# Kernel tuning notes

Measured on AMD Instinct MI355X. Metric: run time of the kernel, lower is better.

The kernel has to match this reference:

```python
import jax, jax.numpy as jnp
import numpy as np

N_NODES = 50000
N_EDGES = 1600000
D_FEAT = 64
N_SCALARS = 4
N_GRAPHS = 64
HIDDEN = 128
OUT = 128


def setup_inputs() -> dict:
    key = jax.random.key(0)
    ks = jax.random.split(key, 8)
    x = jax.random.normal(ks[0], (N_NODES, D_FEAT), dtype=jnp.float32)
    scalars = jax.random.normal(ks[1], (N_GRAPHS, N_SCALARS), dtype=jnp.float32)
    batch = jnp.sort(jax.random.randint(ks[2], (N_NODES,), 0, N_GRAPHS))
    edge_index = jax.random.randint(ks[3], (2, N_EDGES), 0, N_NODES)
    d_in = 2 * (D_FEAT + N_SCALARS)  # 136: EdgeConv-style cat([x_i, x_j - x_i])
    W1 = jax.random.normal(ks[4], (d_in, HIDDEN), dtype=jnp.float32) * (1.0 / np.sqrt(d_in))
    b1 = jnp.zeros((HIDDEN,), dtype=jnp.float32)
    W2 = jax.random.normal(ks[5], (HIDDEN, OUT), dtype=jnp.float32) * (1.0 / np.sqrt(HIDDEN))
    b2 = jnp.zeros((OUT,), dtype=jnp.float32)
    return {"x": x, "scalars": scalars, "batch": batch, "edge_index": edge_index,
            "W1": W1, "b1": b1, "W2": W2, "b2": b2}


def reference(x, scalars, batch, edge_index, W1, b1, W2, b2):
    # _reshape_scalars: gather per-graph scalars to nodes via batch index
    s = scalars[batch]                       # [N, n_scalars]
    h = jnp.concatenate([x, s], axis=-1)     # [N, d_feat + n_scalars]
    src, dst = edge_index[0], edge_index[1]  # edge j -> i (PyG convention)
    h_i = h[dst]                             # target node features [E, F]
    h_j = h[src]                             # source node features [E, F]
    m_in = jnp.concatenate([h_i, h_j - h_i], axis=-1)  # [E, 2F]
    m = jax.nn.relu(m_in @ W1 + b1) @ W2 + b2          # edge MLP [E, OUT]
    out = jax.ops.segment_sum(m, dst, num_segments=x.shape[0])  # add-aggregation
    return out
```

## Files before the change

### kernel.cpp

```cpp
#include <hip/hip_runtime.h>

#define N_NODES   50000
#define N_EDGES   1600000
#define D_FEAT    64
#define N_SCALARS 4
#define HIDDEN    128
#define OUT_DIM   128
#define UV_DIM    256

#define SLICE_SH  6
#define SLICE_N   (1 << SLICE_SH)
#define NSLICE    ((N_NODES + SLICE_N - 1) >> SLICE_SH)
#define CAP       2560
#define DEGMAX    80
#define CAPN      96
#define CAPN_DW   (CAPN / 2)
#define CHUNK     4096
#define SENTINEL  50000

#define N_WAVES   (N_NODES / 16)
#define G1_BLOCKS ((N_WAVES + 3) / 4)
#define BIN_BLOCKS ((N_EDGES + CHUNK - 1) / CHUNK)
#define AGG_BLOCKS (N_NODES / 16)

typedef __attribute__((ext_vector_type(8))) _Float16 half8;
typedef __attribute__((ext_vector_type(2))) _Float16 half2v;
typedef __attribute__((ext_vector_type(4))) float    f32x4;

__device__ __forceinline__ float wf_elem(const float* W1, int k, int j) {
    float wb = W1[(k + 68) * HIDDEN + (j & 127)];
    return (j < HIDDEN) ? (W1[k * HIDDEN + j] - wb) : wb;
}

__device__ __forceinline__ unsigned char f2bf8(float f) {
    unsigned short h = __builtin_bit_cast(unsigned short, (_Float16)f);
    unsigned r = ((unsigned)h + 0x7Fu + ((h >> 8) & 1u)) >> 8;
    return (unsigned char)r;
}

__device__ __forceinline__ half2v bf8lo(unsigned v) {
    return __builtin_bit_cast(half2v, __builtin_amdgcn_perm(0u, v, 0x010C000Cu));
}
__device__ __forceinline__ half2v bf8hi(unsigned v) {
    return __builtin_bit_cast(half2v, __builtin_amdgcn_perm(0u, v, 0x030C020Cu));
}
__device__ __forceinline__ half2v h2bc(unsigned v) {
    return __builtin_bit_cast(half2v, v);
}
__device__ __forceinline__ unsigned h2u(half2v v) {
    return __builtin_bit_cast(unsigned, v);
}

__global__ __launch_bounds__(256) void prep_kernel(
    const float* __restrict__ W1, const float* __restrict__ b1,
    const float* __restrict__ W2, const float* __restrict__ scalars,
    _Float16* __restrict__ WfT, _Float16* __restrict__ W2T,
    float* __restrict__ SG, int* __restrict__ tails,
    unsigned char* __restrict__ Vb8)
{
    const int idx = blockIdx.x * 256 + threadIdx.x;
    {   int j = idx >> 6, k = idx & 63;
        WfT[idx] = (_Float16)wf_elem(W1, k, j); }
    {   int j = idx >> 7, k = idx & 127;
        W2T[idx] = (_Float16)W2[k * OUT_DIM + j]; }
    {   int g = idx >> 8, j = idx & 255;
        float s = (j < HIDDEN) ? b1[j] : 0.f;
        #pragma unroll
        for (int t = 0; t < N_SCALARS; ++t)
            s = fmaf(scalars[g * N_SCALARS + t], wf_elem(W1, D_FEAT + t, j), s);
        SG[idx] = s; }
    if (idx < NSLICE) tails[idx] = 0;
    if (idx < 32)
        ((unsigned*)(Vb8 + (size_t)SENTINEL * HIDDEN))[idx] = 0xFCFCFCFCu;
}

__global__ __launch_bounds__(256) void gemm1_bin(
    const float* __restrict__ x, const int* __restrict__ batch,
    const _Float16* __restrict__ WfT, const float* __restrict__ SG,
    _Float16* __restrict__ Uh, unsigned char* __restrict__ Vb8,
    const int* __restrict__ ei, int* __restrict__ tails,
    unsigned* __restrict__ glist)
{
    __shared__ unsigned buf[CHUNK];
    __shared__ int hist[NSLICE];
    __shared__ int binStart[NSLICE];
    __shared__ int cursor[NSLICE];
    __shared__ int gbase[NSLICE];
    __shared__ int scanTmp[256];

    const int tid = threadIdx.x;

    if (blockIdx.x < G1_BLOCKS) {
        const int wid = (blockIdx.x * 256 + tid) >> 6;
        if (wid >= N_WAVES) return;
        const int lane = tid & 63;
        const int quad = lane >> 4;
        const int l15  = lane & 15;
        const int row0 = wid * 16;

        f32x4 acc[16];
        #pragma unroll
        for (int c = 0; c < 16; ++c) { f32x4 z = {0.f,0.f,0.f,0.f}; acc[c] = z; }

        const float* xrow = x + (row0 + l15) * D_FEAT;
        #pragma unroll
        for (int t = 0; t < 2; ++t) {
            const int k0 = 32 * t + quad * 8;
            float4 a0 = *(const float4*)(xrow + k0);
            float4 a1 = *(const float4*)(xrow + k0 + 4);
            half8 af;
            af[0] = (_Float16)a0.x; af[1] = (_Float16)a0.y;
            af[2] = (_Float16)a0.z; af[3] = (_Float16)a0.w;
            af[4] = (_Float16)a1.x; af[5] = (_Float16)a1.y;
            af[6] = (_Float16)a1.z; af[7] = (_Float16)a1.w;
            #pragma unroll
            for (int c = 0; c < 16; ++c) {
                half8 bf = *(const half8*)(WfT + (c * 16 + l15) * 64 + k0);
                acc[c] = __builtin_amdgcn_mfma_f32_16x16x32_f16(af, bf, acc[c], 0, 0, 0);
            }
        }

        const int gA = batch[row0];
        const int gB = batch[row0 + 15];

        if (gA == gB) {
            const float* SGr = SG + gA * UV_DIM;
            #pragma unroll
            for (int c = 0; c < 16; ++c) {
                const int col = c * 16 + l15;
                const float sg = SGr[col];
                #pragma unroll
                for (int j = 0; j < 4; ++j) {
                    const int n = row0 + quad * 4 + j;
                    float v = acc[c][j] + sg;
                    if (col < HIDDEN) Uh[(n << 7) + col] = (_Float16)v;
                    else              Vb8[(n << 7) + col - HIDDEN] = f2bf8(v);
                }
            }
        } else {
            int bg[4];
            #pragma unroll
            for (int j = 0; j < 4; ++j) bg[j] = batch[row0 + quad * 4 + j];
            #pragma unroll
            for (int c = 0; c < 16; ++c) {
                const int col = c * 16 + l15;
                #pragma unroll
                for (int j = 0; j < 4; ++j) {
                    const int n = row0 + quad * 4 + j;
                    float v = acc[c][j] + SG[bg[j] * UV_DIM + col];
                    if (col < HIDDEN) Uh[(n << 7) + col] = (_Float16)v;
                    else              Vb8[(n << 7) + col - HIDDEN] = f2bf8(v);
                }
            }
        }
        return;
    }

    const int e0  = (blockIdx.x - G1_BLOCKS) * CHUNK;
    const int nE  = min(CHUNK, N_EDGES - e0);

    for (int i = tid; i < NSLICE; i += 256) hist[i] = 0;
    __syncthreads();

    unsigned ent[CHUNK / 256];
    #pragma unroll
    for (int j = 0; j < CHUNK / 256; ++j) {
        int e = e0 + tid + j * 256;
        if (e < N_EDGES) {
            unsigned s = (unsigned)ei[e];
            unsigned d = (unsigned)ei[N_EDGES + e];
            ent[j] = (d << 16) | s;
            atomicAdd(&hist[d >> SLICE_SH], 1);
        } else {
            ent[j] = 0xFFFFFFFFu;
        }
    }
    __syncthreads();

    const int base4 = tid * 4;
    int loc[4];
    int sum = 0;
    #pragma unroll
    for (int k = 0; k < 4; ++k) {
        int b = base4 + k;
        loc[k] = (b < NSLICE) ? hist[b] : 0;
        sum += loc[k];
    }
    scanTmp[tid] = sum;
    __syncthreads();
    for (int d = 1; d < 256; d <<= 1) {
        int v = (tid >= d) ? scanTmp[tid - d] : 0;
        __syncthreads();
        scanTmp[tid] += v;
        __syncthreads();
    }
    int run = (tid == 0) ? 0 : scanTmp[tid - 1];
    #pragma unroll
    for (int k = 0; k < 4; ++k) {
        int b = base4 + k;
        if (b < NSLICE) { binStart[b] = run; cursor[b] = run; run += loc[k]; }
    }
    __syncthreads();

    #pragma unroll
    for (int j = 0; j < CHUNK / 256; ++j) {
        if (ent[j] != 0xFFFFFFFFu) {
            int sl = (int)(ent[j] >> (16 + SLICE_SH));
            int pos = atomicAdd(&cursor[sl], 1);
            buf[pos] = ent[j];
        }
    }
    __syncthreads();

    for (int s = tid; s < NSLICE; s += 256) {
        int c = hist[s];
        if (c > 0) gbase[s] = atomicAdd(&tails[s], c);
    }
    __syncthreads();

    for (int i = tid; i < nE; i += 256) {
        unsigned e = buf[i];
        int sl = (int)(e >> (16 + SLICE_SH));
        int di = gbase[sl] + (i - binStart[sl]);
        if (di < CAP) glist[(size_t)sl * CAP + di] = e;
    }
}

__global__ __launch_bounds__(256) void rebin_kernel(
    const unsigned* __restrict__ glist, const int* __restrict__ tails,
    unsigned short* __restrict__ nlist, int* __restrict__ degN)
{
    __shared__ unsigned short lists[64 * CAPN];
    __shared__ int cur[64];

    const int sl  = blockIdx.x;
    const int tid = threadIdx.x;
    const unsigned* lst = glist + (size_t)sl * CAP;
    const int cnt = min(tails[sl], CAP);

    unsigned* L32 = (unsigned*)lists;
    #pragma unroll
    for (int k = 0; k < (64 * CAPN_DW) / 256; ++k)
        L32[tid + k * 256] = (SENTINEL << 16) | SENTINEL;
    if (tid < 64) cur[tid] = 0;
    __syncthreads();

    for (int i = tid; i < cnt; i += 256) {
        unsigned e = lst[i];
        int b = (e >> 16) & 63;
        int pos = atomicAdd(&cur[b], 1);
        if (pos < DEGMAX) lists[b * CAPN + pos] = (unsigned short)e;
    }
    __syncthreads();

    unsigned* N32 = (unsigned*)nlist + (size_t)sl * (64 * CAPN_DW);
    #pragma unroll
    for (int k = 0; k < (64 * CAPN_DW) / 256; ++k)
        N32[tid + k * 256] = L32[tid + k * 256];

    if (tid < 64) degN[sl * 64 + tid] = min(cur[tid], DEGMAX);
}

__global__ __launch_bounds__(512, 8) void agg_gemm2(
    const unsigned short* __restrict__ nlist, const int* __restrict__ degN,
    const _Float16* __restrict__ Uh, const unsigned char* __restrict__ Vb8,
    const _Float16* __restrict__ W2T, const float* __restrict__ b2,
    float* __restrict__ out)
{
    __shared__ _Float16 aggA[16][136];
    __shared__ int deg16[16];

    const int node0 = blockIdx.x << 4;
    const int tid   = threadIdx.x;
    const int wave  = tid >> 6;
    const int lane  = tid & 63;
    const int g     = lane >> 3;
    const int co    = (lane & 7) * 16;
    const half2v zero = {(_Float16)0, (_Float16)0};

    if (tid < 16) deg16[tid] = min(degN[node0 + tid], DEGMAX);

    const int n0 = node0 + wave * 2;
    const int d0 = min(degN[n0], DEGMAX);
    const int d1 = min(degN[n0 + 1], DEGMAX);
    const int nch = (max(d0, d1) + 7) >> 3;

    const unsigned char* Vbc = Vb8 + co;
    const unsigned short* L0 = nlist + (size_t)n0 * CAPN + g;
    const unsigned short* L1 = L0 + CAPN;

    half2v U0[8], U1[8], A0[8], A1[8];
    {
        const _Float16* up = Uh + (((size_t)n0) << 7) + co;
        uint4 a = *(const uint4*)up;
        uint4 b = *(const uint4*)(up + 8);
        U0[0] = h2bc(a.x); U0[1] = h2bc(a.y);
        U0[2] = h2bc(a.z); U0[3] = h2bc(a.w);
        U0[4] = h2bc(b.x); U0[5] = h2bc(b.y);
        U0[6] = h2bc(b.z); U0[7] = h2bc(b.w);
        uint4 c = *(const uint4*)(up + 128);
        uint4 d = *(const uint4*)(up + 136);
        U1[0] = h2bc(c.x); U1[1] = h2bc(c.y);
        U1[2] = h2bc(c.z); U1[3] = h2bc(c.w);
        U1[4] = h2bc(d.x); U1[5] = h2bc(d.y);
        U1[6] = h2bc(d.z); U1[7] = h2bc(d.w);
        #pragma unroll
        for (int k = 0; k < 8; ++k) { A0[k] = zero; A1[k] = zero; }
    }

    unsigned s0c = L0[0], s1c = L1[0];
    unsigned s0n = L0[8], s1n = L1[8];
    uint4 v0 = *(const uint4*)(Vbc + ((size_t)s0c << 7));
    uint4 v1 = *(const uint4*)(Vbc + ((size_t)s1c << 7));

    for (int ch = 0; ch < nch; ++ch) {
        uint4 v0n = *(const uint4*)(Vbc + ((size_t)s0n << 7));
        uint4 v1n = *(const uint4*)(Vbc + ((size_t)s1n << 7));
        s0n = L0[(ch + 2) * 8];
        s1n = L1[(ch + 2) * 8];

        A0[0] += __builtin_elementwise_max(U0[0] + bf8lo(v0.x), zero);
        A0[1] += __builtin_elementwise_max(U0[1] + bf8hi(v0.x), zero);
        A0[2] += __builtin_elementwise_max(U0[2] + bf8lo(v0.y), zero);
        A0[3] += __builtin_elementwise_max(U0[3] + bf8hi(v0.y), zero);
        A0[4] += __builtin_elementwise_max(U0[4] + bf8lo(v0.z), zero);
        A0[5] += __builtin_elementwise_max(U0[5] + bf8hi(v0.z), zero);
        A0[6] += __builtin_elementwise_max(U0[6] + bf8lo(v0.w), zero);
        A0[7] += __builtin_elementwise_max(U0[7] + bf8hi(v0.w), zero);
        A1[0] += __builtin_elementwise_max(U1[0] + bf8lo(v1.x), zero);
        A1[1] += __builtin_elementwise_max(U1[1] + bf8hi(v1.x), zero);
        A1[2] += __builtin_elementwise_max(U1[2] + bf8lo(v1.y), zero);
        A1[3] += __builtin_elementwise_max(U1[3] + bf8hi(v1.y), zero);
        A1[4] += __builtin_elementwise_max(U1[4] + bf8lo(v1.z), zero);
        A1[5] += __builtin_elementwise_max(U1[5] + bf8hi(v1.z), zero);
        A1[6] += __builtin_elementwise_max(U1[6] + bf8lo(v1.w), zero);
        A1[7] += __builtin_elementwise_max(U1[7] + bf8hi(v1.w), zero);

        v0 = v0n; v1 = v1n;
    }

    #pragma unroll
    for (int k = 0; k < 8; ++k) {
        half2v t0 = A0[k];
        t0 += h2bc((unsigned)__shfl_xor((int)h2u(t0), 8));
        t0 += h2bc((unsigned)__shfl_xor((int)h2u(t0), 16));
        t0 += h2bc((unsigned)__shfl_xor((int)h2u(t0), 32));
        A0[k] = t0;
        half2v t1 = A1[k];
        t1 += h2bc((unsigned)__shfl_xor((int)h2u(t1), 8));
        t1 += h2bc((unsigned)__shfl_xor((int)h2u(t1), 16));
        t1 += h2bc((unsigned)__shfl_xor((int)h2u(t1), 32));
        A1[k] = t1;
    }

    if (lane < 8) {
        _Float16* dst0 = &aggA[wave * 2][co];
        uint4 w0 = { h2u(A0[0]), h2u(A0[1]), h2u(A0[2]), h2u(A0[3]) };
        uint4 w1 = { h2u(A0[4]), h2u(A0[5]), h2u(A0[6]), h2u(A0[7]) };
        *(uint4*)dst0 = w0;
        *(uint4*)(dst0 + 8) = w1;
        _Float16* dst1 = &aggA[wave * 2 + 1][co];
        uint4 w2 = { h2u(A1[0]), h2u(A1[1]), h2u(A1[2]), h2u(A1[3]) };
        uint4 w3 = { h2u(A1[4]), h2u(A1[5]), h2u(A1[6]), h2u(A1[7]) };
        *(uint4*)dst1 = w2;
        *(uint4*)(dst1 + 8) = w3;
    }
    __syncthreads();

    const int quad = lane >> 4;
    const int l15  = lane & 15;
    f32x4 accm = {0.f, 0.f, 0.f, 0.f};
    #pragma unroll
    for (int t = 0; t < 4; ++t) {
        const int k0 = 32 * t + quad * 8;
        half8 af = *(const half8*)&aggA[l15][k0];
        half8 bf = *(const half8*)(W2T + ((wave * 16 + l15) << 7) + k0);
        accm = __builtin_amdgcn_mfma_f32_16x16x32_f16(af, bf, accm, 0, 0, 0);
    }
    int dgj[4];
    #pragma unroll
    for (int j = 0; j < 4; ++j) dgj[j] = deg16[quad * 4 + j];

    const int col = wave * 16 + l15;
    const float bb = b2[col];
    #pragma unroll
    for (int j = 0; j < 4; ++j) {
        const int n = node0 + quad * 4 + j;
        out[(size_t)n * OUT_DIM + col] = accm[j] + bb * (float)dgj[j];
    }
}

extern "C" void kernel_launch(void* const* d_in, const int* in_sizes, int n_in,
                              void* d_out, int out_size, void* d_ws, size_t ws_size,
                              hipStream_t stream)
{
    const float* x       = (const float*)d_in[0];
    const float* scalars = (const float*)d_in[1];
    const int*   batch   = (const int*)d_in[2];
    const int*   ei      = (const int*)d_in[3];
    const float* W1      = (const float*)d_in[4];
    const float* b1      = (const float*)d_in[5];
    const float* W2      = (const float*)d_in[6];
    const float* b2      = (const float*)d_in[7];
    float*       out     = (float*)d_out;

    _Float16*       Uh    = (_Float16*)d_ws;
    unsigned char*  Vb8   = (unsigned char*)(Uh + (size_t)N_NODES * HIDDEN);
    unsigned*       glist = (unsigned*)(Vb8 + (size_t)(N_NODES + 1) * HIDDEN);
    unsigned short* nlist = (unsigned short*)(glist + (size_t)NSLICE * CAP);
    int*            degN  = (int*)(nlist + (size_t)NSLICE * SLICE_N * CAPN);
    _Float16*       WfT   = (_Float16*)(degN + NSLICE * SLICE_N);
    _Float16*       W2T   = WfT + 256 * 64;
    float*          SG    = (float*)(W2T + 128 * 128);
    int*            tails = (int*)(SG + 64 * UV_DIM);

    prep_kernel<<<64, 256, 0, stream>>>(W1, b1, W2, scalars, WfT, W2T, SG, tails, Vb8);

    gemm1_bin<<<G1_BLOCKS + BIN_BLOCKS, 256, 0, stream>>>(
        x, batch, WfT, SG, Uh, Vb8, ei, tails, glist);

    rebin_kernel<<<NSLICE, 256, 0, stream>>>(glist, tails, nlist, degN);

    agg_gemm2<<<AGG_BLOCKS, 512, 0, stream>>>(
        nlist, degN, Uh, Vb8, W2T, b2, out);
}
```

Baseline: 166.1 us.

## Replace global atomic slice tails with per-block staged buckets and histograms

The binning blocks now write each locally sorted chunk straight to a staging buffer, along with per-block histograms and bin starts, instead of reserving space through global atomics on per-slice tails and scattering into fixed-capacity slice lists. The rebin kernel then walks every binning block's segment for its slice. This removes the global atomics, the tails reset and the scattered writes, in exchange for rebin reading a 391x782 metadata matrix and doing short serial per-thread segment loops with poor coalescing. It also drops the CAP overflow truncation, and the resulting edge order can differ.

Result: slower. 172.7 us (+4.0%).

```diff
diff --git a/kernel.cpp b/kernel.cpp
--- a/kernel.cpp
+++ b/kernel.cpp
@@ -11,7 +11,6 @@
 #define SLICE_SH  6
 #define SLICE_N   (1 << SLICE_SH)
 #define NSLICE    ((N_NODES + SLICE_N - 1) >> SLICE_SH)
-#define CAP       2560
 #define DEGMAX    80
 #define CAPN      96
 #define CAPN_DW   (CAPN / 2)
@@ -55,8 +54,7 @@
     const float* __restrict__ W1, const float* __restrict__ b1,
     const float* __restrict__ W2, const float* __restrict__ scalars,
     _Float16* __restrict__ WfT, _Float16* __restrict__ W2T,
-    float* __restrict__ SG, int* __restrict__ tails,
-    unsigned char* __restrict__ Vb8)
+    float* __restrict__ SG, unsigned char* __restrict__ Vb8)
 {
     const int idx = blockIdx.x * 256 + threadIdx.x;
     {   int j = idx >> 6, k = idx & 63;
@@ -69,7 +67,6 @@
         for (int t = 0; t < N_SCALARS; ++t)
             s = fmaf(scalars[g * N_SCALARS + t], wf_elem(W1, D_FEAT + t, j), s);
         SG[idx] = s; }
-    if (idx < NSLICE) tails[idx] = 0;
     if (idx < 32)
         ((unsigned*)(Vb8 + (size_t)SENTINEL * HIDDEN))[idx] = 0xFCFCFCFCu;
 }
@@ -78,14 +75,13 @@
     const float* __restrict__ x, const int* __restrict__ batch,
     const _Float16* __restrict__ WfT, const float* __restrict__ SG,
     _Float16* __restrict__ Uh, unsigned char* __restrict__ Vb8,
-    const int* __restrict__ ei, int* __restrict__ tails,
-    unsigned* __restrict__ glist)
+    const int* __restrict__ ei, unsigned* __restrict__ gstage,
+    int* __restrict__ histM, int* __restrict__ startM)
 {
     __shared__ unsigned buf[CHUNK];
     __shared__ int hist[NSLICE];
     __shared__ int binStart[NSLICE];
     __shared__ int cursor[NSLICE];
-    __shared__ int gbase[NSLICE];
     __shared__ int scanTmp[256];
 
     const int tid = threadIdx.x;
@@ -156,8 +152,8 @@
         return;
     }
 
-    const int e0  = (blockIdx.x - G1_BLOCKS) * CHUNK;
-    const int nE  = min(CHUNK, N_EDGES - e0);
+    const int bb  = blockIdx.x - G1_BLOCKS;
+    const int e0  = bb * CHUNK;
 
     for (int i = tid; i < NSLICE; i += 256) hist[i] = 0;
     __syncthreads();
@@ -212,22 +208,19 @@
     }
     __syncthreads();
 
+    unsigned* gs = gstage + (size_t)bb * CHUNK;
+    #pragma unroll
+    for (int j = 0; j < CHUNK / 256; ++j)
+        gs[tid + j * 256] = buf[tid + j * 256];
     for (int s = tid; s < NSLICE; s += 256) {
-        int c = hist[s];
-        if (c > 0) gbase[s] = atomicAdd(&tails[s], c);
-    }
-    __syncthreads();
-
-    for (int i = tid; i < nE; i += 256) {
-        unsigned e = buf[i];
-        int sl = (int)(e >> (16 + SLICE_SH));
-        int di = gbase[sl] + (i - binStart[sl]);
-        if (di < CAP) glist[(size_t)sl * CAP + di] = e;
+        histM [(size_t)bb * NSLICE + s] = hist[s];
+        startM[(size_t)bb * NSLICE + s] = binStart[s];
     }
 }
 
 __global__ __launch_bounds__(256) void rebin_kernel(
-    const unsigned* __restrict__ glist, const int* __restrict__ tails,
+    const unsigned* __restrict__ gstage, const int* __restrict__ histM,
+    const int* __restrict__ startM,
     unsigned short* __restrict__ nlist, int* __restrict__ degN)
 {
     __shared__ unsigned short lists[64 * CAPN];
@@ -235,8 +228,6 @@
 
     const int sl  = blockIdx.x;
     const int tid = threadIdx.x;
-    const unsigned* lst = glist + (size_t)sl * CAP;
-    const int cnt = min(tails[sl], CAP);
 
     unsigned* L32 = (unsigned*)lists;
     #pragma unroll
@@ -245,11 +236,17 @@
     if (tid < 64) cur[tid] = 0;
     __syncthreads();
 
-    for (int i = tid; i < cnt; i += 256) {
-        unsigned e = lst[i];
-        int b = (e >> 16) & 63;
-        int pos = atomicAdd(&cur[b], 1);
-        if (pos < DEGMAX) lists[b * CAPN + pos] = (unsigned short)e;
+    for (int b = tid; b < BIN_BLOCKS; b += 256) {
+        const int len = histM[(size_t)b * NSLICE + sl];
+        if (len <= 0) continue;
+        const unsigned* seg = gstage + (size_t)b * CHUNK
+                            + startM[(size_t)b * NSLICE + sl];
+        for (int i = 0; i < len; ++i) {
+            unsigned e = seg[i];
+            int nd = (e >> 16) & 63;
+            int pos = atomicAdd(&cur[nd], 1);
+            if (pos < DEGMAX) lists[nd * CAPN + pos] = (unsigned short)e;
+        }
     }
     __syncthreads();
 
@@ -404,22 +401,23 @@
     const float* b2      = (const float*)d_in[7];
     float*       out     = (float*)d_out;
 
-    _Float16*       Uh    = (_Float16*)d_ws;
-    unsigned char*  Vb8   = (unsigned char*)(Uh + (size_t)N_NODES * HIDDEN);
-    unsigned*       glist = (unsigned*)(Vb8 + (size_t)(N_NODES + 1) * HIDDEN);
-    unsigned short* nlist = (unsigned short*)(glist + (size_t)NSLICE * CAP);
-    int*            degN  = (int*)(nlist + (size_t)NSLICE * SLICE_N * CAPN);
-    _Float16*       WfT   = (_Float16*)(degN + NSLICE * SLICE_N);
-    _Float16*       W2T   = WfT + 256 * 64;
-    float*          SG    = (float*)(W2T + 128 * 128);
-    int*            tails = (int*)(SG + 64 * UV_DIM);
-
-    prep_kernel<<<64, 256, 0, stream>>>(W1, b1, W2, scalars, WfT, W2T, SG, tails, Vb8);
+    _Float16*       Uh     = (_Float16*)d_ws;
+    unsigned char*  Vb8    = (unsigned char*)(Uh + (size_t)N_NODES * HIDDEN);
+    unsigned*       gstage = (unsigned*)(Vb8 + (size_t)(N_NODES + 1) * HIDDEN);
+    unsigned short* nlist  = (unsigned short*)(gstage + (size_t)BIN_BLOCKS * CHUNK);
+    int*            degN   = (int*)(nlist + (size_t)NSLICE * SLICE_N * CAPN);
+    int*            histM  = degN + NSLICE * SLICE_N;
+    int*            startM = histM + (size_t)BIN_BLOCKS * NSLICE;
+    _Float16*       WfT    = (_Float16*)(startM + (size_t)BIN_BLOCKS * NSLICE);
+    _Float16*       W2T    = WfT + 256 * 64;
+    float*          SG     = (float*)(W2T + 128 * 128);
+
+    prep_kernel<<<64, 256, 0, stream>>>(W1, b1, W2, scalars, WfT, W2T, SG, Vb8);
 
     gemm1_bin<<<G1_BLOCKS + BIN_BLOCKS, 256, 0, stream>>>(
-        x, batch, WfT, SG, Uh, Vb8, ei, tails, glist);
-
-    rebin_kernel<<<NSLICE, 256, 0, stream>>>(glist, tails, nlist, degN);
+        x, batch, WfT, SG, Uh, Vb8, ei, gstage, histM, startM);
+
+    rebin_kernel<<<NSLICE, 256, 0, stream>>>(gstage, histM, startM, nlist, degN);
 
     agg_gemm2<<<AGG_BLOCKS, 512, 0, stream>>>(
         nlist, degN, Uh, Vb8, W2T, b2, out);
```

## Split edge aggregation into two column-half passes to shrink gather working set

Applied to the files above, without the earlier changes.

The aggregation kernel is split into two launches. Each one gathers only 64 of the 128 hidden columns of the fp8 V table per neighbour, and the first pass stores its partial aggregate to a workspace buffer that the second pass reads back before the GEMM2 MFMA. The aim is to halve the random-gather footprint of Vb8 per pass so each half stays cache-resident. In exchange it adds an extra kernel launch, reads the neighbour lists and degrees twice, writes and reads back an intermediate buffer, and issues narrower 8-byte gathers.

Result: slower. 192.4 us (+15.8%).

```diff
diff --git a/kernel.cpp b/kernel.cpp
--- a/kernel.cpp
+++ b/kernel.cpp
@@ -261,61 +261,46 @@
     if (tid < 64) degN[sl * 64 + tid] = min(cur[tid], DEGMAX);
 }
 
-__global__ __launch_bounds__(512, 8) void agg_gemm2(
+template<int H>
+__device__ __forceinline__ void agg_gather_half(
     const unsigned short* __restrict__ nlist, const int* __restrict__ degN,
     const _Float16* __restrict__ Uh, const unsigned char* __restrict__ Vb8,
-    const _Float16* __restrict__ W2T, const float* __restrict__ b2,
-    float* __restrict__ out)
-{
-    __shared__ _Float16 aggA[16][136];
-    __shared__ int deg16[16];
-
-    const int node0 = blockIdx.x << 4;
-    const int tid   = threadIdx.x;
-    const int wave  = tid >> 6;
-    const int lane  = tid & 63;
-    const int g     = lane >> 3;
-    const int co    = (lane & 7) * 16;
+    int node0, int wave, int lane, half2v A0[4], half2v A1[4])
+{
+    const int g  = lane >> 3;
+    const int co = (lane & 7) * 8;
     const half2v zero = {(_Float16)0, (_Float16)0};
-
-    if (tid < 16) deg16[tid] = min(degN[node0 + tid], DEGMAX);
 
     const int n0 = node0 + wave * 2;
     const int d0 = min(degN[n0], DEGMAX);
     const int d1 = min(degN[n0 + 1], DEGMAX);
     const int nch = (max(d0, d1) + 7) >> 3;
 
-    const unsigned char* Vbc = Vb8 + co;
+    const unsigned char* Vbc = Vb8 + H * 64 + co;
     const unsigned short* L0 = nlist + (size_t)n0 * CAPN + g;
     const unsigned short* L1 = L0 + CAPN;
 
-    half2v U0[8], U1[8], A0[8], A1[8];
+    half2v U0[4], U1[4];
     {
-        const _Float16* up = Uh + (((size_t)n0) << 7) + co;
+        const _Float16* up = Uh + (((size_t)n0) << 7) + H * 64 + co;
         uint4 a = *(const uint4*)up;
-        uint4 b = *(const uint4*)(up + 8);
         U0[0] = h2bc(a.x); U0[1] = h2bc(a.y);
         U0[2] = h2bc(a.z); U0[3] = h2bc(a.w);
-        U0[4] = h2bc(b.x); U0[5] = h2bc(b.y);
-        U0[6] = h2bc(b.z); U0[7] = h2bc(b.w);
         uint4 c = *(const uint4*)(up + 128);
-        uint4 d = *(const uint4*)(up + 136);
         U1[0] = h2bc(c.x); U1[1] = h2bc(c.y);
         U1[2] = h2bc(c.z); U1[3] = h2bc(c.w);
-        U1[4] = h2bc(d.x); U1[5] = h2bc(d.y);
-        U1[6] = h2bc(d.z); U1[7] = h2bc(d.w);
         #pragma unroll
-        for (int k = 0; k < 8; ++k) { A0[k] = zero; A1[k] = zero; }
+        for (int k = 0; k < 4; ++k) { A0[k] = zero; A1[k] = zero; }
     }
 
     unsigned s0c = L0[0], s1c = L1[0];
     unsigned s0n = L0[8], s1n = L1[8];
-    uint4 v0 = *(const uint4*)(Vbc + ((size_t)s0c << 7));
-    uint4 v1 = *(const uint4*)(Vbc + ((size_t)s1c << 7));
+    uint2 v0 = *(const uint2*)(Vbc + ((size_t)s0c << 7));
+    uint2 v1 = *(const uint2*)(Vbc + ((size_t)s1c << 7));
 
     for (int ch = 0; ch < nch; ++ch) {
-        uint4 v0n = *(const uint4*)(Vbc + ((size_t)s0n << 7));
-        uint4 v1n = *(const uint4*)(Vbc + ((size_t)s1n << 7));
+        uint2 v0n = *(const uint2*)(Vbc + ((size_t)s0n << 7));
+        uint2 v1n = *(const uint2*)(Vbc + ((size_t)s1n << 7));
         s0n = L0[(ch + 2) * 8];
         s1n = L1[(ch + 2) * 8];
 
@@ -323,24 +308,16 @@
         A0[1] += __builtin_elementwise_max(U0[1] + bf8hi(v0.x), zero);
         A0[2] += __builtin_elementwise_max(U0[2] + bf8lo(v0.y), zero);
         A0[3] += __builtin_elementwise_max(U0[3] + bf8hi(v0.y), zero);
-        A0[4] += __builtin_elementwise_max(U0[4] + bf8lo(v0.z), zero);
-        A0[5] += __builtin_elementwise_max(U0[5] + bf8hi(v0.z), zero);
-        A0[6] += __builtin_elementwise_max(U0[6] + bf8lo(v0.w), zero);
-        A0[7] += __builtin_elementwise_max(U0[7] + bf8hi(v0.w), zero);
         A1[0] += __builtin_elementwise_max(U1[0] + bf8lo(v1.x), zero);
         A1[1] += __builtin_elementwise_max(U1[1] + bf8hi(v1.x), zero);
         A1[2] += __builtin_elementwise_max(U1[2] + bf8lo(v1.y), zero);
         A1[3] += __builtin_elementwise_max(U1[3] + bf8hi(v1.y), zero);
-        A1[4] += __builtin_elementwise_max(U1[4] + bf8lo(v1.z), zero);
-        A1[5] += __builtin_elementwise_max(U1[5] + bf8hi(v1.z), zero);
-        A1[6] += __builtin_elementwise_max(U1[6] + bf8lo(v1.w), zero);
-        A1[7] += __builtin_elementwise_max(U1[7] + bf8hi(v1.w), zero);
 
         v0 = v0n; v1 = v1n;
     }
 
     #pragma unroll
-    for (int k = 0; k < 8; ++k) {
+    for (int k = 0; k < 4; ++k) {
         half2v t0 = A0[k];
         t0 += h2bc((unsigned)__shfl_xor((int)h2u(t0), 8));
         t0 += h2bc((unsigned)__shfl_xor((int)h2u(t0), 16));
@@ -352,18 +329,62 @@
         t1 += h2bc((unsigned)__shfl_xor((int)h2u(t1), 32));
         A1[k] = t1;
     }
+}
+
+__global__ __launch_bounds__(512, 8) void agg_pass1(
+    const unsigned short* __restrict__ nlist, const int* __restrict__ degN,
+    const _Float16* __restrict__ Uh, const unsigned char* __restrict__ Vb8,
+    _Float16* __restrict__ Pagg)
+{
+    const int node0 = blockIdx.x << 4;
+    const int tid   = threadIdx.x;
+    const int wave  = tid >> 6;
+    const int lane  = tid & 63;
+
+    half2v A0[4], A1[4];
+    agg_gather_half<0>(nlist, degN, Uh, Vb8, node0, wave, lane, A0, A1);
 
     if (lane < 8) {
-        _Float16* dst0 = &aggA[wave * 2][co];
+        const int n0 = node0 + wave * 2;
+        const int co = (lane & 7) * 8;
         uint4 w0 = { h2u(A0[0]), h2u(A0[1]), h2u(A0[2]), h2u(A0[3]) };
-        uint4 w1 = { h2u(A0[4]), h2u(A0[5]), h2u(A0[6]), h2u(A0[7]) };
-        *(uint4*)dst0 = w0;
-        *(uint4*)(dst0 + 8) = w1;
-        _Float16* dst1 = &aggA[wave * 2 + 1][co];
-        uint4 w2 = { h2u(A1[0]), h2u(A1[1]), h2u(A1[2]), h2u(A1[3]) };
-        uint4 w3 = { h2u(A1[4]), h2u(A1[5]), h2u(A1[6]), h2u(A1[7]) };
-        *(uint4*)dst1 = w2;
-        *(uint4*)(dst1 + 8) = w3;
+        uint4 w1 = { h2u(A1[0]), h2u(A1[1]), h2u(A1[2]), h2u(A1[3]) };
+        *(uint4*)(Pagg + (size_t)n0 * 64 + co) = w0;
+        *(uint4*)(Pagg + (size_t)(n0 + 1) * 64 + co) = w1;
+    }
+}
+
+__global__ __launch_bounds__(512, 8) void agg_pass2(
+    const unsigned short* __restrict__ nlist, const int* __restrict__ degN,
+    const _Float16* __restrict__ Uh, const unsigned char* __restrict__ Vb8,
+    const _Float16* __restrict__ Pagg,
+    const _Float16* __restrict__ W2T, const float* __restrict__ b2,
+    float* __restrict__ out)
+{
+    __shared__ _Float16 aggA[16][136];
+    __shared__ int deg16[16];
+
+    const int node0 = blockIdx.x << 4;
+    const int tid   = threadIdx.x;
+    const int wave  = tid >> 6;
+    const int lane  = tid & 63;
+
+    if (tid < 16) deg16[tid] = min(degN[node0 + tid], DEGMAX);
+
+    half2v A0[4], A1[4];
+    agg_gather_half<1>(nlist, degN, Uh, Vb8, node0, wave, lane, A0, A1);
+
+    if (lane < 8) {
+        const int n0 = node0 + wave * 2;
+        const int co = (lane & 7) * 8;
+        uint4 w0 = { h2u(A0[0]), h2u(A0[1]), h2u(A0[2]), h2u(A0[3]) };
+        uint4 w1 = { h2u(A1[0]), h2u(A1[1]), h2u(A1[2]), h2u(A1[3]) };
+        *(uint4*)&aggA[wave * 2][64 + co] = w0;
+        *(uint4*)&aggA[wave * 2 + 1][64 + co] = w1;
+        uint4 p0 = *(const uint4*)(Pagg + (size_t)n0 * 64 + co);
+        uint4 p1 = *(const uint4*)(Pagg + (size_t)(n0 + 1) * 64 + co);
+        *(uint4*)&aggA[wave * 2][co] = p0;
+        *(uint4*)&aggA[wave * 2 + 1][co] = p1;
     }
     __syncthreads();
 
@@ -409,7 +430,8 @@
     unsigned*       glist = (unsigned*)(Vb8 + (size_t)(N_NODES + 1) * HIDDEN);
     unsigned short* nlist = (unsigned short*)(glist + (size_t)NSLICE * CAP);
     int*            degN  = (int*)(nlist + (size_t)NSLICE * SLICE_N * CAPN);
-    _Float16*       WfT   = (_Float16*)(degN + NSLICE * SLICE_N);
+    _Float16*       Pagg  = (_Float16*)(degN + NSLICE * SLICE_N);
+    _Float16*       WfT   = Pagg + (size_t)N_NODES * 64;
     _Float16*       W2T   = WfT + 256 * 64;
     float*          SG    = (float*)(W2T + 128 * 128);
     int*            tails = (int*)(SG + 64 * UV_DIM);
@@ -421,6 +443,8 @@
 
     rebin_kernel<<<NSLICE, 256, 0, stream>>>(glist, tails, nlist, degN);
 
-    agg_gemm2<<<AGG_BLOCKS, 512, 0, stream>>>(
-        nlist, degN, Uh, Vb8, W2T, b2, out);
-}
+    agg_pass1<<<AGG_BLOCKS, 512, 0, stream>>>(nlist, degN, Uh, Vb8, Pagg);
+
+    agg_pass2<<<AGG_BLOCKS, 512, 0, stream>>>(
+        nlist, degN, Uh, Vb8, Pagg, W2T, b2, out);
+}
```

## Split aggregation into two source-range passes for L2 locality of V gathers

Applied to the files above, without the earlier changes.

The rebin kernel now splits each node's neighbor list into a low-source half (src < 25000) and a high-source half, padded to chunk boundaries, and records both degrees. Aggregation runs as two kernels: pass A gathers only the low-half V rows and writes fp16 partial sums to a new workspace buffer, and pass B gathers the high half, adds the partials and does the second GEMM. Each pass touches only half the V table, which is meant to keep the random gathers resident in cache. The cost is an extra launch, a second edge-list scan in rebin, extra chunk padding and the write and read of a fp16 partial-sum buffer. The bin CHUNK size is also doubled.

Result: slower. 191.8 us (+15.5%).

```diff
diff --git a/kernel.cpp b/kernel.cpp
--- a/kernel.cpp
+++ b/kernel.cpp
@@ -15,8 +15,9 @@
 #define DEGMAX    80
 #define CAPN      96
 #define CAPN_DW   (CAPN / 2)
-#define CHUNK     4096
+#define CHUNK     8192
 #define SENTINEL  50000
+#define SRC_HALF  25000
 
 #define N_WAVES   (N_NODES / 16)
 #define G1_BLOCKS ((N_WAVES + 3) / 4)
@@ -228,10 +229,13 @@
 
 __global__ __launch_bounds__(256) void rebin_kernel(
     const unsigned* __restrict__ glist, const int* __restrict__ tails,
-    unsigned short* __restrict__ nlist, int* __restrict__ degN)
+    unsigned short* __restrict__ nlist, int* __restrict__ degN,
+    int* __restrict__ degLoN)
 {
     __shared__ unsigned short lists[64 * CAPN];
     __shared__ int cur[64];
+    __shared__ int lo64[64];
+    __shared__ int base64[64];
 
     const int sl  = blockIdx.x;
     const int tid = threadIdx.x;
@@ -247,9 +251,27 @@
 
     for (int i = tid; i < cnt; i += 256) {
         unsigned e = lst[i];
-        int b = (e >> 16) & 63;
-        int pos = atomicAdd(&cur[b], 1);
-        if (pos < DEGMAX) lists[b * CAPN + pos] = (unsigned short)e;
+        if ((e & 0xFFFFu) < SRC_HALF) {
+            int b = (e >> 16) & 63;
+            int pos = atomicAdd(&cur[b], 1);
+            if (pos < DEGMAX) lists[b * CAPN + pos] = (unsigned short)e;
+        }
+    }
+    __syncthreads();
+    if (tid < 64) {
+        int lo = min(cur[tid], DEGMAX);
+        lo64[tid]   = lo;
+        base64[tid] = (lo + 7) & ~7;
+        cur[tid]    = base64[tid];
+    }
+    __syncthreads();
+    for (int i = tid; i < cnt; i += 256) {
+        unsigned e = lst[i];
+        if ((e & 0xFFFFu) >= SRC_HALF) {
+            int b = (e >> 16) & 63;
+            int pos = atomicAdd(&cur[b], 1);
+            if (pos < CAPN) lists[b * CAPN + pos] = (unsigned short)e;
+        }
     }
     __syncthreads();
 
@@ -258,66 +280,47 @@
     for (int k = 0; k < (64 * CAPN_DW) / 256; ++k)
         N32[tid + k * 256] = L32[tid + k * 256];
 
-    if (tid < 64) degN[sl * 64 + tid] = min(cur[tid], DEGMAX);
-}
-
-__global__ __launch_bounds__(512, 8) void agg_gemm2(
-    const unsigned short* __restrict__ nlist, const int* __restrict__ degN,
-    const _Float16* __restrict__ Uh, const unsigned char* __restrict__ Vb8,
-    const _Float16* __restrict__ W2T, const float* __restrict__ b2,
-    float* __restrict__ out)
-{
-    __shared__ _Float16 aggA[16][136];
-    __shared__ int deg16[16];
-
-    const int node0 = blockIdx.x << 4;
-    const int tid   = threadIdx.x;
-    const int wave  = tid >> 6;
-    const int lane  = tid & 63;
-    const int g     = lane >> 3;
-    const int co    = (lane & 7) * 16;
+    if (tid < 64) {
+        int lo = lo64[tid];
+        int hi = min(cur[tid], CAPN) - base64[tid];
+        degLoN[sl * 64 + tid] = lo;
+        degN  [sl * 64 + tid] = lo + hi;
+    }
+}
+
+__device__ __forceinline__ unsigned sid_at(
+    const unsigned short* L, int base, int nchN, int c)
+{
+    int cc = min(c, max(nchN - 1, 0));
+    unsigned v = L[base + cc * 8];
+    return (c < nchN) ? v : (unsigned)SENTINEL;
+}
+
+__device__ __forceinline__ void agg_gather_seg(
+    const unsigned short* L0, const unsigned short* L1,
+    int base0, int cnt0, int base1, int cnt1,
+    const unsigned char* Vbc,
+    const half2v U0[8], const half2v U1[8],
+    half2v A0[8], half2v A1[8])
+{
     const half2v zero = {(_Float16)0, (_Float16)0};
-
-    if (tid < 16) deg16[tid] = min(degN[node0 + tid], DEGMAX);
-
-    const int n0 = node0 + wave * 2;
-    const int d0 = min(degN[n0], DEGMAX);
-    const int d1 = min(degN[n0 + 1], DEGMAX);
-    const int nch = (max(d0, d1) + 7) >> 3;
-
-    const unsigned char* Vbc = Vb8 + co;
-    const unsigned short* L0 = nlist + (size_t)n0 * CAPN + g;
-    const unsigned short* L1 = L0 + CAPN;
-
-    half2v U0[8], U1[8], A0[8], A1[8];
-    {
-        const _Float16* up = Uh + (((size_t)n0) << 7) + co;
-        uint4 a = *(const uint4*)up;
-        uint4 b = *(const uint4*)(up + 8);
-        U0[0] = h2bc(a.x); U0[1] = h2bc(a.y);
-        U0[2] = h2bc(a.z); U0[3] = h2bc(a.w);
-        U0[4] = h2bc(b.x); U0[5] = h2bc(b.y);
-        U0[6] = h2bc(b.z); U0[7] = h2bc(b.w);
-        uint4 c = *(const uint4*)(up + 128);
-        uint4 d = *(const uint4*)(up + 136);
-        U1[0] = h2bc(c.x); U1[1] = h2bc(c.y);
-        U1[2] = h2bc(c.z); U1[3] = h2bc(c.w);
-        U1[4] = h2bc(d.x); U1[5] = h2bc(d.y);
-        U1[6] = h2bc(d.z); U1[7] = h2bc(d.w);
-        #pragma unroll
-        for (int k = 0; k < 8; ++k) { A0[k] = zero; A1[k] = zero; }
-    }
-
-    unsigned s0c = L0[0], s1c = L1[0];
-    unsigned s0n = L0[8], s1n = L1[8];
+    const int nch0 = (cnt0 + 7) >> 3;
+    const int nch1 = (cnt1 + 7) >> 3;
+    const int nch  = max(nch0, nch1);
+    if (nch == 0) return;
+
+    unsigned s0c = sid_at(L0, base0, nch0, 0);
+    unsigned s1c = sid_at(L1, base1, nch1, 0);
+    unsigned s0n = sid_at(L0, base0, nch0, 1);
+    unsigned s1n = sid_at(L1, base1, nch1, 1);
     uint4 v0 = *(const uint4*)(Vbc + ((size_t)s0c << 7));
     uint4 v1 = *(const uint4*)(Vbc + ((size_t)s1c << 7));
 
     for (int ch = 0; ch < nch; ++ch) {
         uint4 v0n = *(const uint4*)(Vbc + ((size_t)s0n << 7));
         uint4 v1n = *(const uint4*)(Vbc + ((size_t)s1n << 7));
-        s0n = L0[(ch + 2) * 8];
-        s1n = L1[(ch + 2) * 8];
+        s0n = sid_at(L0, base0, nch0, ch + 2);
+        s1n = sid_at(L1, base1, nch1, ch + 2);
 
         A0[0] += __builtin_elementwise_max(U0[0] + bf8lo(v0.x), zero);
         A0[1] += __builtin_elementwise_max(U0[1] + bf8hi(v0.x), zero);
@@ -338,7 +341,10 @@
 
         v0 = v0n; v1 = v1n;
     }
-
+}
+
+__device__ __forceinline__ void agg_reduce8(half2v A0[8], half2v A1[8])
+{
     #pragma unroll
     for (int k = 0; k < 8; ++k) {
         half2v t0 = A0[k];
@@ -352,8 +358,127 @@
         t1 += h2bc((unsigned)__shfl_xor((int)h2u(t1), 32));
         A1[k] = t1;
     }
+}
+
+__device__ __forceinline__ void agg_load_u(
+    const _Float16* __restrict__ Uh, int n0, int co,
+    half2v U0[8], half2v U1[8])
+{
+    const _Float16* up = Uh + (((size_t)n0) << 7) + co;
+    uint4 a = *(const uint4*)up;
+    uint4 b = *(const uint4*)(up + 8);
+    U0[0] = h2bc(a.x); U0[1] = h2bc(a.y);
+    U0[2] = h2bc(a.z); U0[3] = h2bc(a.w);
+    U0[4] = h2bc(b.x); U0[5] = h2bc(b.y);
+    U0[6] = h2bc(b.z); U0[7] = h2bc(b.w);
+    uint4 c = *(const uint4*)(up + 128);
+    uint4 d = *(const uint4*)(up + 136);
+    U1[0] = h2bc(c.x); U1[1] = h2bc(c.y);
+    U1[2] = h2bc(c.z); U1[3] = h2bc(c.w);
+    U1[4] = h2bc(d.x); U1[5] = h2bc(d.y);
+    U1[6] = h2bc(d.z); U1[7] = h2bc(d.w);
+}
+
+__global__ __launch_bounds__(512, 8) void agg_passA(
+    const unsigned short* __restrict__ nlist, const int* __restrict__ degLoN,
+    const _Float16* __restrict__ Uh, const unsigned char* __restrict__ Vb8,
+    _Float16* __restrict__ Pagg)
+{
+    const int node0 = blockIdx.x << 4;
+    const int tid   = threadIdx.x;
+    const int wave  = tid >> 6;
+    const int lane  = tid & 63;
+    const int g     = lane >> 3;
+    const int co    = (lane & 7) * 16;
+    const half2v zero = {(_Float16)0, (_Float16)0};
+
+    const int n0  = node0 + wave * 2;
+    const int lo0 = degLoN[n0];
+    const int lo1 = degLoN[n0 + 1];
+
+    const unsigned short* L0 = nlist + (size_t)n0 * CAPN + g;
+    const unsigned short* L1 = L0 + CAPN;
+    const unsigned char*  Vbc = Vb8 + co;
+
+    half2v U0[8], U1[8], A0[8], A1[8];
+    agg_load_u(Uh, n0, co, U0, U1);
+    #pragma unroll
+    for (int k = 0; k < 8; ++k) { A0[k] = zero; A1[k] = zero; }
+
+    agg_gather_seg(L0, L1, 0, lo0, 0, lo1, Vbc, U0, U1, A0, A1);
+    agg_reduce8(A0, A1);
 
     if (lane < 8) {
+        _Float16* dst0 = Pagg + (size_t)n0 * 128 + co;
+        uint4 w0 = { h2u(A0[0]), h2u(A0[1]), h2u(A0[2]), h2u(A0[3]) };
+        uint4 w1 = { h2u(A0[4]), h2u(A0[5]), h2u(A0[6]), h2u(A0[7]) };
+        *(uint4*)dst0 = w0;
+        *(uint4*)(dst0 + 8) = w1;
+        _Float16* dst1 = dst0 + 128;
+        uint4 w2 = { h2u(A1[0]), h2u(A1[1]), h2u(A1[2]), h2u(A1[3]) };
+        uint4 w3 = { h2u(A1[4]), h2u(A1[5]), h2u(A1[6]), h2u(A1[7]) };
+        *(uint4*)dst1 = w2;
+        *(uint4*)(dst1 + 8) = w3;
+    }
+}
+
+__global__ __launch_bounds__(512, 8) void agg_passB(
+    const unsigned short* __restrict__ nlist, const int* __restrict__ degN,
+    const int* __restrict__ degLoN,
+    const _Float16* __restrict__ Uh, const unsigned char* __restrict__ Vb8,
+    const _Float16* __restrict__ Pagg,
+    const _Float16* __restrict__ W2T, const float* __restrict__ b2,
+    float* __restrict__ out)
+{
+    __shared__ _Float16 aggA[16][136];
+    __shared__ int deg16[16];
+
+    const int node0 = blockIdx.x << 4;
+    const int tid   = threadIdx.x;
+    const int wave  = tid >> 6;
+    const int lane  = tid & 63;
+    const int g     = lane >> 3;
+    const int co    = (lane & 7) * 16;
+    const half2v zero = {(_Float16)0, (_Float16)0};
+
+    if (tid < 16) deg16[tid] = min(degN[node0 + tid], DEGMAX);
+
+    const int n0  = node0 + wave * 2;
+    const int lo0 = degLoN[n0];
+    const int lo1 = degLoN[n0 + 1];
+    const int hb0 = (lo0 + 7) & ~7;
+    const int hb1 = (lo1 + 7) & ~7;
+    const int hi0 = degN[n0]     - lo0;
+    const int hi1 = degN[n0 + 1] - lo1;
+
+    const unsigned short* L0 = nlist + (size_t)n0 * CAPN + g;
+    const unsigned short* L1 = L0 + CAPN;
+    const unsigned char*  Vbc = Vb8 + co;
+
+    half2v U0[8], U1[8], A0[8], A1[8];
+    agg_load_u(Uh, n0, co, U0, U1);
+    #pragma unroll
+    for (int k = 0; k < 8; ++k) { A0[k] = zero; A1[k] = zero; }
+
+    agg_gather_seg(L0, L1, hb0, hi0, hb1, hi1, Vbc, U0, U1, A0, A1);
+    agg_reduce8(A0, A1);
+
+    if (lane < 8) {
+        const _Float16* p0 = Pagg + (size_t)n0 * 128 + co;
+        uint4 pa = *(const uint4*)p0;
+        uint4 pb = *(const uint4*)(p0 + 8);
+        A0[0] += h2bc(pa.x); A0[1] += h2bc(pa.y);
+        A0[2] += h2bc(pa.z); A0[3] += h2bc(pa.w);
+        A0[4] += h2bc(pb.x); A0[5] += h2bc(pb.y);
+        A0[6] += h2bc(pb.z); A0[7] += h2bc(pb.w);
+        const _Float16* p1 = p0 + 128;
+        uint4 pc = *(const uint4*)p1;
+        uint4 pd = *(const uint4*)(p1 + 8);
+        A1[0] += h2bc(pc.x); A1[1] += h2bc(pc.y);
+        A1[2] += h2bc(pc.z); A1[3] += h2bc(pc.w);
+        A1[4] += h2bc(pd.x); A1[5] += h2bc(pd.y);
+        A1[6] += h2bc(pd.z); A1[7] += h2bc(pd.w);
+
         _Float16* dst0 = &aggA[wave * 2][co];
         uint4 w0 = { h2u(A0[0]), h2u(A0[1]), h2u(A0[2]), h2u(A0[3]) };
         uint4 w1 = { h2u(A0[4]), h2u(A0[5]), h2u(A0[6]), h2u(A0[7]) };
@@ -404,23 +529,27 @@
     const float* b2      = (const float*)d_in[7];
     float*       out     = (float*)d_out;
 
-    _Float16*       Uh    = (_Float16*)d_ws;
-    unsigned char*  Vb8   = (unsigned char*)(Uh + (size_t)N_NODES * HIDDEN);
-    unsigned*       glist = (unsigned*)(Vb8 + (size_t)(N_NODES + 1) * HIDDEN);
-    unsigned short* nlist = (unsigned short*)(glist + (size_t)NSLICE * CAP);
-    int*            degN  = (int*)(nlist + (size_t)NSLICE * SLICE_N * CAPN);
-    _Float16*       WfT   = (_Float16*)(degN + NSLICE * SLICE_N);
-    _Float16*       W2T   = WfT + 256 * 64;
-    float*          SG    = (float*)(W2T + 128 * 128);
-    int*            tails = (int*)(SG + 64 * UV_DIM);
+    _Float16*       Uh     = (_Float16*)d_ws;
+    unsigned char*  Vb8    = (unsigned char*)(Uh + (size_t)N_NODES * HIDDEN);
+    unsigned*       glist  = (unsigned*)(Vb8 + (size_t)(N_NODES + 1) * HIDDEN);
+    unsigned short* nlist  = (unsigned short*)(glist + (size_t)NSLICE * CAP);
+    int*            degN   = (int*)(nlist + (size_t)NSLICE * SLICE_N * CAPN);
+    int*            degLoN = degN + NSLICE * SLICE_N;
+    _Float16*       Pagg   = (_Float16*)(degLoN + NSLICE * SLICE_N);
+    _Float16*       WfT    = Pagg + (size_t)N_NODES * 128;
+    _Float16*       W2T    = WfT + 256 * 64;
+    float*          SG     = (float*)(W2T + 128 * 128);
+    int*            tails  = (int*)(SG + 64 * UV_DIM);
 
     prep_kernel<<<64, 256, 0, stream>>>(W1, b1, W2, scalars, WfT, W2T, SG, tails, Vb8);
 
     gemm1_bin<<<G1_BLOCKS + BIN_BLOCKS, 256, 0, stream>>>(
         x, batch, WfT, SG, Uh, Vb8, ei, tails, glist);
 
-    rebin_kernel<<<NSLICE, 256, 0, stream>>>(glist, tails, nlist, degN);
-
-    agg_gemm2<<<AGG_BLOCKS, 512, 0, stream>>>(
-        nlist, degN, Uh, Vb8, W2T, b2, out);
-}
+    rebin_kernel<<<NSLICE, 256, 0, stream>>>(glist, tails, nlist, degN, degLoN);
+
+    agg_passA<<<AGG_BLOCKS, 512, 0, stream>>>(nlist, degLoN, Uh, Vb8, Pagg);
+
+    agg_passB<<<AGG_BLOCKS, 512, 0, stream>>>(
+        nlist, degN, degLoN, Uh, Vb8, Pagg, W2T, b2, out);
+}
```
